# Optimization experiments

Hardware: AMD Instinct MI355X
Metric: run time of the kernel (lower is better)

## Reference

```python
import jax, jax.numpy as jnp
import numpy as np

N_E = 1024
E_DIM = 256
N_TOK = 65536
BETA = 0.25


def setup_inputs() -> dict:
    key = jax.random.key(0)
    k1, k2 = jax.random.split(key)
    z = jax.random.normal(k1, (N_TOK, E_DIM), dtype=jnp.float32)
    # nn.Embedding weight, init uniform(-1/n_e, 1/n_e) in the original; use normal-like scale via uniform
    W = jax.random.uniform(k2, (N_E, E_DIM), dtype=jnp.float32, minval=-1.0 / N_E, maxval=1.0 / N_E)
    return {"z": z, "W": W}


def reference(z, W):
    # cosine distance: d = -normalize(z) @ normalize(W).T  -> (N, n_e)
    zn = z / jnp.linalg.norm(z, axis=-1, keepdims=True)
    Wn = W / jnp.linalg.norm(W, axis=-1, keepdims=True)
    d = -jnp.einsum('nd,ed->ne', zn, Wn)
    min_idx = jnp.argmin(d, axis=1)                       # (N,)
    z_q = W[min_idx]                                       # (N, e_dim)
    # commitment / codebook loss with straight-through style detaches
    loss = jnp.mean((jax.lax.stop_gradient(z) - z_q) ** 2) \
         + BETA * jnp.mean((z - jax.lax.stop_gradient(z_q)) ** 2)
    # pos_indices = unique(min_idx) (sorted); neg = np.delete(arange(n_e), pos) (sorted)
    # emb = cat(W[pos], W[neg]); reproduce with a stable argsort on membership mask
    pos_mask = jnp.zeros((N_E,), dtype=bool).at[min_idx].set(True)
    order = jnp.argsort(jnp.logical_not(pos_mask), stable=True)  # pos (sorted) first, then neg (sorted)
    emb = W[order]                                         # (n_e, e_dim)
    label = pos_mask[order].astype(z.dtype)                # (n_e,)
    return emb, label, loss
```

## Files before the change

### kernel.cpp

```cpp
#include <hip/hip_runtime.h>
#include <hip/hip_bf16.h>
#include <hip/hip_fp16.h>
#include <math.h>


typedef unsigned short u16;
typedef unsigned int   u32;
typedef unsigned long long u64;
typedef __attribute__((ext_vector_type(8))) _Float16 f16x8;
typedef __attribute__((ext_vector_type(4))) float f32x4;

#define N_E   1024
#define E_DIM 256
#define N_TOK 65536
#define BETA  0.25f
#define CAPL  24
#define CAPG  8
#define D_ADM 0.025f
#define D_FIL 0.026f

#define WS_INVNORM 0
#define WS_NORMW   4096
#define WS_MASK    8192
#define WS_LACC    12288
#define WS_WCNT    14336
#define WS_WCNT2   14340
#define WS_WSW     16384
#define WS_CNT     540672
#define WS_CAND    802816
#define WS_WLIST   1851392
#define WS_WLIST2  2113536

static __device__ __forceinline__ u32 pk2fh(float a, float b) {
    __half2 p = __float22half2_rn(make_float2(a, b));
    return *reinterpret_cast<u32*>(&p);
}
static __device__ __forceinline__ u32 keyenc(float f) {
    u32 u = __float_as_uint(f);
    return u ^ (u32)(((int)u >> 31) | 0x80000000);
}
static __device__ __forceinline__ float keydec(u32 k) {
    u32 u = (k & 0x80000000u) ? (k ^ 0x80000000u) : ~k;
    return __uint_as_float(u);
}

__global__ void k_prep(const float* __restrict__ W, u16* __restrict__ Wsw,
                       float* __restrict__ inv_norm, float* __restrict__ normW,
                       int* __restrict__ mask, double* __restrict__ lacc,
                       u32* __restrict__ wcnt, u32* __restrict__ wcnt2) {
    const int n = blockIdx.x;
    const int l = threadIdx.x;
    const float4 v = reinterpret_cast<const float4*>(W + (size_t)n * E_DIM)[l];
    float s = v.x * v.x + v.y * v.y + v.z * v.z + v.w * v.w;
#pragma unroll
    for (int sh = 1; sh < 64; sh <<= 1) s += __shfl_xor(s, sh, 64);
    const float nw = sqrtf(s), inv = 1.0f / nw;
    if (l == 0) {
        inv_norm[n] = inv; normW[n] = nw; mask[n] = 0;
        if (n < 256) lacc[n] = 0.0;
        if (n == 0) { *wcnt = 0u; *wcnt2 = 0u; }
    }
    const int o = l >> 1;
    const int kc = o >> 2, q = o & 3;
    const size_t base =
        (((((size_t)(n >> 7) * 8 + kc) * 8 + ((n >> 4) & 7)) * 64 +
          (q * 16 + (n & 15))) * 8) + (l & 1) * 4;
    u32* dst = reinterpret_cast<u32*>(Wsw + base);
    dst[0] = pk2fh(v.x * inv, v.y * inv);
    dst[1] = pk2fh(v.z * inv, v.w * inv);
}

__global__ __launch_bounds__(512, 2)
void k_score(const float* __restrict__ z, const u16* __restrict__ Wsw,
             const float* __restrict__ normW, u16* __restrict__ cand_g,
             u32* __restrict__ cnt_g, int* __restrict__ mask,
             u32* __restrict__ wlist, u32* __restrict__ wcnt,
             u32* __restrict__ wlist2, u32* __restrict__ wcnt2,
             double* __restrict__ lacc) {
    __shared__ __align__(16) u16 A_sw[32768];
    __shared__ u32 bestk[128];
    __shared__ u32 cnt[128];
    __shared__ u32 slots[128 * CAPL];

    const int t    = threadIdx.x;
    const int lane = t & 63;
    const int w    = t >> 6;
    const size_t tok_base = (size_t)blockIdx.x * 128;

    if (t < 128) { bestk[t] = 0u; cnt[t] = 0u; }

    float ssq = 0.f;
#pragma unroll
    for (int i = 0; i < 8; i++) {
        const int m = ((i & 1) << 6) | (w << 3) | (lane & 7);
        const int o = ((i >> 1) << 3) | (lane >> 3);
        const float* zp = z + (tok_base + m) * E_DIM + o * 8;
        const float4 v0 = reinterpret_cast<const float4*>(zp)[0];
        const float4 v1 = reinterpret_cast<const float4*>(zp)[1];
        ssq += v0.x * v0.x + v0.y * v0.y + v0.z * v0.z + v0.w * v0.w
             + v1.x * v1.x + v1.y * v1.y + v1.z * v1.z + v1.w * v1.w;
        uint4 d;
        d.x = pk2fh(v0.x, v0.y);
        d.y = pk2fh(v0.z, v0.w);
        d.z = pk2fh(v1.x, v1.y);
        d.w = pk2fh(v1.z, v1.w);
        const int kc = o >> 2, q = o & 3, col = m & 15, mt = m >> 4;
        *reinterpret_cast<uint4*>(A_sw + ((size_t)((kc * 8 + mt) * 64 + q * 16 + col)) * 8) = d;
    }
#pragma unroll
    for (int sh = 1; sh < 64; sh <<= 1) ssq += __shfl_xor(ssq, sh, 64);
    if (lane == 0) atomicAdd(&lacc[(blockIdx.x * 8 + w) & 255], (double)ssq);
    __syncthreads();

    const int mq = w >> 2;
    const int nq = w & 3;
    const int q = lane >> 4, col = lane & 15;
    const u16* wb = Wsw + ((size_t)((nq >> 1) * 64 + (nq & 1) * 4)) * 512
                        + (size_t)lane * 8;

    f32x4 acc[4][4];

#define ZERO_ACC() { _Pragma("unroll") for (int mi = 0; mi < 4; mi++) \
    _Pragma("unroll") for (int ni = 0; ni < 4; ni++) { \
        f32x4 zf = {0.f, 0.f, 0.f, 0.f}; acc[mi][ni] = zf; } }

#define KLOOP(NB2) { \
    __builtin_amdgcn_s_setprio(1); \
    _Pragma("unroll") \
    for (int kc = 0; kc < 8; kc++) { \
        f16x8 bf[4], af[4]; \
        _Pragma("unroll") for (int ni = 0; ni < 4; ni++) \
            bf[ni] = *reinterpret_cast<const f16x8*>( \
                wb + (size_t)((NB2) * 128 + kc * 8 + ni) * 512); \
        _Pragma("unroll") for (int mi = 0; mi < 4; mi++) \
            af[mi] = *reinterpret_cast<const f16x8*>( \
                A_sw + ((size_t)((kc * 8 + mq * 4 + mi) * 64 + lane)) * 8); \
        _Pragma("unroll") for (int mi = 0; mi < 4; mi++) \
        _Pragma("unroll") for (int ni = 0; ni < 4; ni++) \
            acc[mi][ni] = __builtin_amdgcn_mfma_f32_16x16x32_f16( \
                af[mi], bf[ni], acc[mi][ni], 0, 0, 0); } \
    __builtin_amdgcn_s_setprio(0); }

#define ADMIT(NB2, DO_MAX) { \
    _Pragma("unroll") for (int mi = 0; mi < 4; mi++) \
    _Pragma("unroll") for (int r = 0; r < 4; r++) { \
        const int tk = mq * 64 + mi * 16 + q * 4 + r; \
        const float thr = keydec(bestk[tk]) - D_ADM; \
        const float vmax = fmaxf(fmaxf(acc[mi][0][r], acc[mi][1][r]), \
                                 fmaxf(acc[mi][2][r], acc[mi][3][r])); \
        if (vmax >= thr) { \
            if (DO_MAX) atomicMax(&bestk[tk], keyenc(vmax)); \
            _Pragma("unroll") for (int ni = 0; ni < 4; ni++) { \
                const float v = acc[mi][ni][r]; \
                if (v >= thr) { \
                    const int code = ((NB2) * 16 + nq * 4 + ni) * 16 + col; \
                    const u32 sl = atomicAdd(&cnt[tk], 1u); \
                    if (sl < CAPL) { \
                        const float vc = fminf(fmaxf((v + 16.f) * 2048.f, 0.f), 65535.f); \
                        slots[tk * CAPL + sl] = ((u32)vc << 16) | (u32)code; \
                    } } } } } }

    ZERO_ACC();
    KLOOP(0);
#pragma unroll
    for (int mi = 0; mi < 4; mi++)
#pragma unroll
        for (int r = 0; r < 4; r++) {
            float m0 = fmaxf(fmaxf(acc[mi][0][r], acc[mi][1][r]),
                             fmaxf(acc[mi][2][r], acc[mi][3][r]));
#pragma unroll
            for (int sh = 1; sh < 16; sh <<= 1)
                m0 = fmaxf(m0, __shfl_xor(m0, sh, 64));
            if (col == 0)
                atomicMax(&bestk[mq * 64 + mi * 16 + q * 4 + r], keyenc(m0));
        }
    __syncthreads();
    ADMIT(0, 0);

#pragma unroll 1
    for (int nb2 = 1; nb2 < 4; nb2++) {
        ZERO_ACC();
        KLOOP(nb2);
        ADMIT(nb2, 1);
    }
#undef ZERO_ACC
#undef KLOOP
#undef ADMIT

    __syncthreads();
    if (t < 128) {
        const size_t tokg = tok_base + t;
        const u32 c = cnt[t];
        const float best = keydec(bestk[t]);
        bool amb = false, ovf = false;
        float xacc = 0.f;
        if (c > CAPL) {
            ovf = true;
        } else {
            const float thrf = best - D_FIL;
            u16 loc[CAPG]; u32 m = 0;
            for (u32 i = 0; i < c; i++) {
                const u32 s2 = slots[t * CAPL + i];
                const float ap = (float)(s2 >> 16) * (1.0f / 2048.0f) - 16.0f;
                if (ap >= thrf) { if (m < CAPG) loc[m] = (u16)(s2 & 0xFFFFu); m++; }
            }
            if (m == 1) {
                const int bi = loc[0];
                mask[bi] = 1;
                const float nw = normW[bi];
                xacc = fmaf(-2.0f * best, nw, nw * nw);
            } else if (m <= CAPG) {
                for (u32 i = 0; i < m; i++) cand_g[tokg * CAPG + i] = loc[i];
                cnt_g[tokg] = m; amb = true;
            } else {
                ovf = true;
            }
        }
        {
            const u64 bal = __ballot(amb);
            u32 base = 0;
            if (lane == 0 && bal) base = atomicAdd(wcnt, (u32)__popcll(bal));
            base = (u32)__shfl((int)base, 0, 64);
            if (amb) wlist[base + (u32)__popcll(bal & ((1ull << lane) - 1ull))] = (u32)tokg;
        }
        {
            const u64 bal = __ballot(ovf);
            u32 base = 0;
            if (lane == 0 && bal) base = atomicAdd(wcnt2, (u32)__popcll(bal));
            base = (u32)__shfl((int)base, 0, 64);
            if (ovf) wlist2[base + (u32)__popcll(bal & ((1ull << lane) - 1ull))] = (u32)tokg;
        }
        float xs = xacc;
#pragma unroll
        for (int sh = 1; sh < 64; sh <<= 1) xs += __shfl_xor(xs, sh, 64);
        if (lane == 0) atomicAdd(&lacc[(blockIdx.x * 2 + w) & 255], (double)xs);
    }
}

__global__ __launch_bounds__(256)
void k_pick(const float* __restrict__ z, const float* __restrict__ W,
            const float* __restrict__ inv_norm, const float* __restrict__ normW,
            const u16* __restrict__ cand_g, const u32* __restrict__ cnt_g,
            const u32* __restrict__ wlist, const u32* __restrict__ wcnt,
            const u32* __restrict__ wlist2, const u32* __restrict__ wcnt2,
            int* __restrict__ mask, double* __restrict__ lacc) {
    __shared__ float zrow[E_DIM];
    __shared__ float gbv[16], gbp[16];
    __shared__ int   gbi[16];
    const int t = threadIdx.x, lane = t & 63;
    const int gl = t & 15, grp = t >> 4;

    {
        const u32 total = *wcnt;
        float xs = 0.f;
        for (u32 i = blockIdx.x * 16 + grp; i < total; i += 1024 * 16) {
            const size_t tok = wlist[i];
            float4 zv[4];
#pragma unroll
            for (int j = 0; j < 4; j++)
                zv[j] = reinterpret_cast<const float4*>(z + tok * E_DIM)[j * 16 + gl];
            const int n_it = (int)cnt_g[tok];
            float bv = -3.4e38f, bp = 0.f;
            int bi = 0x7FFFFFFF;
#pragma unroll 1
            for (int k2 = 0; k2 < n_it; k2++) {
                const int c = (int)cand_g[tok * CAPG + k2];
                float p = 0.f;
#pragma unroll
                for (int j = 0; j < 4; j++) {
                    const float4 wv = reinterpret_cast<const float4*>(W + (size_t)c * E_DIM)[j * 16 + gl];
                    p += zv[j].x * wv.x + zv[j].y * wv.y + zv[j].z * wv.z + zv[j].w * wv.w;
                }
#pragma unroll
                for (int sh = 1; sh < 16; sh <<= 1) p += __shfl_xor(p, sh, 64);
                const float s = p * inv_norm[c];
                if (s > bv || (s == bv && c < bi)) { bv = s; bi = c; bp = p; }
            }
            if (gl == 0) {
                mask[bi] = 1;
                xs += fmaf(-2.0f, bp, normW[bi] * normW[bi]);
            }
        }
        xs += __shfl_xor(xs, 16, 64);
        xs += __shfl_xor(xs, 32, 64);
        if (lane == 0) atomicAdd(&lacc[(blockIdx.x * 4 + (t >> 6)) & 255], (double)xs);
    }

    {
        const u32 total2 = *wcnt2;
        for (u32 i = blockIdx.x; i < total2; i += 1024) {
            const size_t tok = wlist2[i];
            __syncthreads();
            zrow[t] = z[tok * E_DIM + t];
            __syncthreads();
            float4 zv[4];
#pragma unroll
            for (int j = 0; j < 4; j++)
                zv[j] = reinterpret_cast<const float4*>(zrow)[j * 16 + gl];
            float bv = -3.4e38f, bp = 0.f;
            int bi = 0x7FFFFFFF;
#pragma unroll 1
            for (int k2 = 0; k2 < 64; k2 += 2) {
                const int c0 = grp * 64 + k2, c1 = c0 + 1;
                float p0 = 0.f, p1 = 0.f;
#pragma unroll
                for (int j = 0; j < 4; j++) {
                    const float4 w0 = reinterpret_cast<const float4*>(W + (size_t)c0 * E_DIM)[j * 16 + gl];
                    const float4 w1 = reinterpret_cast<const float4*>(W + (size_t)c1 * E_DIM)[j * 16 + gl];
                    p0 += zv[j].x * w0.x + zv[j].y * w0.y + zv[j].z * w0.z + zv[j].w * w0.w;
                    p1 += zv[j].x * w1.x + zv[j].y * w1.y + zv[j].z * w1.z + zv[j].w * w1.w;
                }
#pragma unroll
                for (int sh = 1; sh < 16; sh <<= 1) {
                    p0 += __shfl_xor(p0, sh, 64);
                    p1 += __shfl_xor(p1, sh, 64);
                }
                const float s0 = p0 * inv_norm[c0];
                const float s1 = p1 * inv_norm[c1];
                if (s0 > bv || (s0 == bv && c0 < bi)) { bv = s0; bi = c0; bp = p0; }
                if (s1 > bv || (s1 == bv && c1 < bi)) { bv = s1; bi = c1; bp = p1; }
            }
            if (gl == 0) { gbv[grp] = bv; gbi[grp] = bi; gbp[grp] = bp; }
            __syncthreads();
            if (t == 0) {
                float fb = gbv[0], fp = gbp[0];
                int fi = gbi[0];
                for (int g2 = 1; g2 < 16; g2++) {
                    const float v2 = gbv[g2];
                    const int i2 = gbi[g2];
                    if (v2 > fb || (v2 == fb && i2 < fi)) { fb = v2; fi = i2; fp = gbp[g2]; }
                }
                mask[fi] = 1;
                atomicAdd(&lacc[tok & 255],
                          (double)fmaf(-2.0f, fp, normW[fi] * normW[fi]));
            }
        }
    }
}

__global__ __launch_bounds__(256)
void k_emit(const float* __restrict__ W, const int* __restrict__ mask,
            const double* __restrict__ lacc, float* __restrict__ out) {
    __shared__ int    redp[256], redt[256];
    __shared__ double dred[256];
    const int e = blockIdx.x;
    const int t = threadIdx.x;
    const int4 mv = reinterpret_cast<const int4*>(mask)[t];
    const int b = t * 4;
    redt[t] = mv.x + mv.y + mv.z + mv.w;
    redp[t] = (b + 0 < e ? mv.x : 0) + (b + 1 < e ? mv.y : 0) +
              (b + 2 < e ? mv.z : 0) + (b + 3 < e ? mv.w : 0);
    if (e == 0) dred[t] = lacc[t];
    __syncthreads();
#pragma unroll
    for (int s2 = 128; s2 > 0; s2 >>= 1) {
        if (t < s2) {
            redp[t] += redp[t + s2];
            redt[t] += redt[t + s2];
            if (e == 0) dred[t] += dred[t + s2];
        }
        __syncthreads();
    }
    const int prefix = redp[0], total = redt[0];
    const int m = mask[e];
    const int r = m ? prefix : (total + e - prefix);
    out[(size_t)r * E_DIM + t] = W[(size_t)e * E_DIM + t];
    if (t == 0) out[(size_t)N_E * E_DIM + r] = m ? 1.0f : 0.0f;
    if (e == 0 && t == 0) {
        const double mse = dred[0] / (double)((size_t)N_TOK * E_DIM);
        out[(size_t)N_E * E_DIM + N_E] = (float)((1.0 + (double)BETA) * mse);
    }
}

extern "C" void kernel_launch(void* const* d_in, const int* in_sizes, int n_in,
                              void* d_out, int out_size, void* d_ws, size_t ws_size,
                              hipStream_t stream) {
    const float* z = (const float*)d_in[0];
    const float* W = (const float*)d_in[1];
    float* out = (float*)d_out;
    char* ws = (char*)d_ws;

    float*  inv_norm = (float*)(ws + WS_INVNORM);
    float*  normW    = (float*)(ws + WS_NORMW);
    int*    mask     = (int*)(ws + WS_MASK);
    double* lacc     = (double*)(ws + WS_LACC);
    u32*    wcnt     = (u32*)(ws + WS_WCNT);
    u32*    wcnt2    = (u32*)(ws + WS_WCNT2);
    u16*    Wsw      = (u16*)(ws + WS_WSW);
    u32*    cnt      = (u32*)(ws + WS_CNT);
    u16*    cand     = (u16*)(ws + WS_CAND);
    u32*    wlist    = (u32*)(ws + WS_WLIST);
    u32*    wlist2   = (u32*)(ws + WS_WLIST2);

    k_prep <<<N_E, 64, 0, stream>>>(W, Wsw, inv_norm, normW, mask, lacc,
                                    wcnt, wcnt2);
    k_score<<<N_TOK / 128, 512, 0, stream>>>(z, Wsw, normW, cand, cnt, mask,
                                             wlist, wcnt, wlist2, wcnt2, lacc);
    k_pick <<<1024, 256, 0, stream>>>(z, W, inv_norm, normW, cand, cnt,
                                      wlist, wcnt, wlist2, wcnt2, mask, lacc);
    k_emit <<<N_E, 256, 0, stream>>>(W, mask, lacc, out);
}
```

Measured before the change: 160.9 us.

## Stage codebook tiles into LDS with double-buffered async global_load_lds

The normalized codebook layout is reordered so that each 16 KB chunk (one k-slice for 256 codes) is contiguous. The score kernel then prefetches the next chunk into a double-buffered LDS region using global_load_lds while MFMAs run on the current chunk. Before this, each wave read B fragments straight from global memory. The change aims to hide global load latency and share B tiles across the waves of the block. In exchange it adds 32 KB of LDS, which may lower occupancy at 2 blocks per CU, plus a __syncthreads per k-step.

```diff
diff --git a/kernel.cpp b/kernel.cpp
--- a/kernel.cpp
+++ b/kernel.cpp
@@ -62,9 +62,10 @@
     }
     const int o = l >> 1;
     const int kc = o >> 2, q = o & 3;
-    const size_t base =
-        (((((size_t)(n >> 7) * 8 + kc) * 8 + ((n >> 4) & 7)) * 64 +
-          (q * 16 + (n & 15))) * 8) + (l & 1) * 4;
+    const int g  = ((n >> 8) << 3) | kc;
+    const int f  = (((n >> 6) & 3) << 2) | ((n >> 4) & 3);
+    const size_t base = (((size_t)g * 16 + f) * 64 + (q * 16 + (n & 15))) * 8
+                        + (l & 1) * 4;
     u32* dst = reinterpret_cast<u32*>(Wsw + base);
     dst[0] = pk2fh(v.x * inv, v.y * inv);
     dst[1] = pk2fh(v.z * inv, v.w * inv);
@@ -78,6 +79,7 @@
              u32* __restrict__ wlist2, u32* __restrict__ wcnt2,
              double* __restrict__ lacc) {
     __shared__ __align__(16) u16 A_sw[32768];
+    __shared__ __align__(16) u16 B_buf[2][8192];
     __shared__ u32 bestk[128];
     __shared__ u32 cnt[128];
     __shared__ u32 slots[128 * CAPL];
@@ -89,6 +91,17 @@
 
     if (t < 128) { bestk[t] = 0u; cnt[t] = 0u; }
 
+#define STAGE(BUF, G) { \
+    const u16* gsrc = Wsw + (size_t)(G) * 8192 + (size_t)w * 1024 + (size_t)lane * 8; \
+    u16* ldst = &B_buf[BUF][w * 1024]; \
+    __builtin_amdgcn_global_load_lds( \
+        (const __attribute__((address_space(1))) void*)gsrc, \
+        (__attribute__((address_space(3))) void*)ldst, 16, 0, 0); \
+    __builtin_amdgcn_global_load_lds( \
+        (const __attribute__((address_space(1))) void*)(gsrc + 512), \
+        (__attribute__((address_space(3))) void*)(ldst + 512), 16, 0, 0); }
+
+    STAGE(0, 0);
     float ssq = 0.f;
 #pragma unroll
     for (int i = 0; i < 8; i++) {
@@ -115,31 +128,12 @@
     const int mq = w >> 2;
     const int nq = w & 3;
     const int q = lane >> 4, col = lane & 15;
-    const u16* wb = Wsw + ((size_t)((nq >> 1) * 64 + (nq & 1) * 4)) * 512
-                        + (size_t)lane * 8;
 
     f32x4 acc[4][4];
 
 #define ZERO_ACC() { _Pragma("unroll") for (int mi = 0; mi < 4; mi++) \
     _Pragma("unroll") for (int ni = 0; ni < 4; ni++) { \
         f32x4 zf = {0.f, 0.f, 0.f, 0.f}; acc[mi][ni] = zf; } }
-
-#define KLOOP(NB2) { \
-    __builtin_amdgcn_s_setprio(1); \
-    _Pragma("unroll") \
-    for (int kc = 0; kc < 8; kc++) { \
-        f16x8 bf[4], af[4]; \
-        _Pragma("unroll") for (int ni = 0; ni < 4; ni++) \
-            bf[ni] = *reinterpret_cast<const f16x8*>( \
-                wb + (size_t)((NB2) * 128 + kc * 8 + ni) * 512); \
-        _Pragma("unroll") for (int mi = 0; mi < 4; mi++) \
-            af[mi] = *reinterpret_cast<const f16x8*>( \
-                A_sw + ((size_t)((kc * 8 + mq * 4 + mi) * 64 + lane)) * 8); \
-        _Pragma("unroll") for (int mi = 0; mi < 4; mi++) \
-        _Pragma("unroll") for (int ni = 0; ni < 4; ni++) \
-            acc[mi][ni] = __builtin_amdgcn_mfma_f32_16x16x32_f16( \
-                af[mi], bf[ni], acc[mi][ni], 0, 0, 0); } \
-    __builtin_amdgcn_s_setprio(0); }
 
 #define ADMIT(NB2, DO_MAX) { \
     _Pragma("unroll") for (int mi = 0; mi < 4; mi++) \
@@ -161,33 +155,58 @@
                     } } } } } }
 
     ZERO_ACC();
-    KLOOP(0);
-#pragma unroll
-    for (int mi = 0; mi < 4; mi++)
-#pragma unroll
-        for (int r = 0; r < 4; r++) {
-            float m0 = fmaxf(fmaxf(acc[mi][0][r], acc[mi][1][r]),
-                             fmaxf(acc[mi][2][r], acc[mi][3][r]));
-#pragma unroll
-            for (int sh = 1; sh < 16; sh <<= 1)
-                m0 = fmaxf(m0, __shfl_xor(m0, sh, 64));
-            if (col == 0)
-                atomicMax(&bestk[mq * 64 + mi * 16 + q * 4 + r], keyenc(m0));
-        }
-    __syncthreads();
-    ADMIT(0, 0);
-
+    int buf = 0;
 #pragma unroll 1
-    for (int nb2 = 1; nb2 < 4; nb2++) {
-        ZERO_ACC();
-        KLOOP(nb2);
-        ADMIT(nb2, 1);
+    for (int g = 0; g < 32; ++g) {
+        const int nb2 = g >> 3, kc = g & 7;
+        if (g < 31) STAGE(buf ^ 1, g + 1);
+
+        f16x8 bf[4], af[4];
+#pragma unroll
+        for (int ni = 0; ni < 4; ni++)
+            bf[ni] = *reinterpret_cast<const f16x8*>(
+                &B_buf[buf][((nq * 4 + ni) * 64 + lane) * 8]);
+#pragma unroll
+        for (int mi = 0; mi < 4; mi++)
+            af[mi] = *reinterpret_cast<const f16x8*>(
+                A_sw + ((size_t)((kc * 8 + mq * 4 + mi) * 64 + lane)) * 8);
+        __builtin_amdgcn_s_setprio(1);
+#pragma unroll
+        for (int mi = 0; mi < 4; mi++)
+#pragma unroll
+            for (int ni = 0; ni < 4; ni++)
+                acc[mi][ni] = __builtin_amdgcn_mfma_f32_16x16x32_f16(
+                    af[mi], bf[ni], acc[mi][ni], 0, 0, 0);
+        __builtin_amdgcn_s_setprio(0);
+
+        if (kc == 7) {
+            if (nb2 == 0) {
+#pragma unroll
+                for (int mi = 0; mi < 4; mi++)
+#pragma unroll
+                    for (int r = 0; r < 4; r++) {
+                        float m0 = fmaxf(fmaxf(acc[mi][0][r], acc[mi][1][r]),
+                                         fmaxf(acc[mi][2][r], acc[mi][3][r]));
+#pragma unroll
+                        for (int sh = 1; sh < 16; sh <<= 1)
+                            m0 = fmaxf(m0, __shfl_xor(m0, sh, 64));
+                        if (col == 0)
+                            atomicMax(&bestk[mq * 64 + mi * 16 + q * 4 + r], keyenc(m0));
+                    }
+                __syncthreads();
+                ADMIT(0, 0);
+            } else {
+                ADMIT(nb2, 1);
+            }
+            ZERO_ACC();
+        }
+        __syncthreads();
+        buf ^= 1;
     }
 #undef ZERO_ACC
-#undef KLOOP
 #undef ADMIT
-
-    __syncthreads();
+#undef STAGE
+
     if (t < 128) {
         const size_t tokg = tok_base + t;
         const u32 c = cnt[t];
```

Result: slower. 184.4 us (+14.6%).
